# Kernel tuning notes

Measured on AMD Instinct MI355X. Metric: run time of the kernel, lower is better.

Reference implementation:

```python
import jax, jax.numpy as jnp
import numpy as np

NUM_HEADS = 12
HIDDEN = 768
HEAD = HIDDEN // NUM_HEADS
SCALE = HIDDEN ** (-0.5)  # NB: module scales by hidden_dim**-0.5, not head_size**-0.5


def setup_inputs() -> dict:
    key = jax.random.key(0)
    ks = jax.random.split(key, 8)
    B, N = 16, 512
    std = HIDDEN ** (-0.5)
    return {
        "x": jax.random.normal(ks[0], (B, N, HIDDEN), dtype=jnp.float32),
        "encoding_bias": jax.random.normal(ks[1], (B, N, N), dtype=jnp.float32),
        "Wq": jax.random.normal(ks[2], (HIDDEN, HIDDEN), dtype=jnp.float32) * std,
        "Wk": jax.random.normal(ks[3], (HIDDEN, HIDDEN), dtype=jnp.float32) * std,
        "Wv": jax.random.normal(ks[4], (HIDDEN, HIDDEN), dtype=jnp.float32) * std,
        "bv": jax.random.normal(ks[5], (HIDDEN,), dtype=jnp.float32) * 0.01,
        "Wo": jax.random.normal(ks[6], (HIDDEN, HIDDEN), dtype=jnp.float32) * std,
        "bo": jax.random.normal(ks[7], (HIDDEN,), dtype=jnp.float32) * 0.01,
    }


def reference(x, encoding_bias, Wq, Wk, Wv, bv, Wo, bo):
    B, N, _ = x.shape
    # torch nn.Linear: y = x @ W.T (+ b)
    q = (x @ Wq.T).reshape(B, N, NUM_HEADS, HEAD)
    k = (x @ Wk.T).reshape(B, N, NUM_HEADS, HEAD)
    v = (x @ Wv.T + bv).reshape(B, N, NUM_HEADS, HEAD)
    # scores: [B, H, N, N] with additive graph bias broadcast over heads
    a = jnp.einsum("bnhd,bmhd->bhnm", q, k) * SCALE + encoding_bias[:, None, :, :]
    # data-dependent pad mask: rows whose scores are identically zero
    pad_mask = jnp.all(a == 0, axis=-1)  # [B, H, N]
    a = jnp.where(pad_mask[..., None], -jnp.inf, a)
    a = jax.nn.softmax(a, axis=-1)
    a = jnp.nan_to_num(a)  # all -inf rows -> NaN -> 0
    o = jnp.einsum("bhnm,bmhd->bnhd", a, v).reshape(B, N, HIDDEN)
    # dropout is identity in eval mode
    return o @ Wo.T + bo
```

## Files before the change

kernel.cpp:

```cpp
#include <hip/hip_runtime.h>
#include <stdint.h>

typedef unsigned short u16;
typedef unsigned int u32;
typedef __bf16 bf16x8 __attribute__((ext_vector_type(8)));
typedef float f32x4 __attribute__((ext_vector_type(4)));

#define NH 12
#define HD 64
#define SEQ 512
#define BATCH 16
#define HID 768
#define SCALE_Q 0.03608439182435161f

__device__ __forceinline__ u16 f2bf(float f) {
    u32 u = __builtin_bit_cast(u32, f);
    u32 r = (u + 0x7FFFu + ((u >> 16) & 1u)) >> 16;
    return (u16)r;
}
__device__ __forceinline__ float bf2f(u16 h) {
    return __builtin_bit_cast(float, (u32)h << 16);
}

__device__ __forceinline__ void gl2lds16(const u16* g, u16* lds_base) {
    __builtin_amdgcn_global_load_lds(
        (const __attribute__((address_space(1))) u32*)g,
        (__attribute__((address_space(3))) u32*)lds_base, 16, 0, 0);
}

#define NXB 6144
#define NEB 4096
#define NWB 576
__global__ void cvt_all(const float* __restrict__ x, const float* __restrict__ eb,
                        const float* __restrict__ w0, const float* __restrict__ w1,
                        const float* __restrict__ w2, const float* __restrict__ w3,
                        u16* __restrict__ dst) {
    int b = blockIdx.x;
    const float* s; int sb;
    if (b < NXB) { s = x; sb = 0; }
    else if (b < NXB + NEB) { s = eb; sb = NXB; }
    else if (b < NXB + NEB + NWB) { s = w0; sb = NXB + NEB; }
    else if (b < NXB + NEB + 2 * NWB) { s = w1; sb = NXB + NEB + NWB; }
    else if (b < NXB + NEB + 3 * NWB) { s = w2; sb = NXB + NEB + 2 * NWB; }
    else { s = w3; sb = NXB + NEB + 3 * NWB; }
    int li = (b - sb) * 1024 + threadIdx.x * 4;
    float4 v = *(const float4*)(s + li);
    ushort4 o;
    o.x = f2bf(v.x); o.y = f2bf(v.y); o.z = f2bf(v.z); o.w = f2bf(v.w);
    *(ushort4*)(dst + (size_t)b * 1024 + threadIdx.x * 4) = o;
}

__device__ __forceinline__ void stage_gemm(
    const u16* __restrict__ Ag, const u16* __restrict__ Bg, int k0,
    u16* As, u16* Bs, int r0, int q0, int r1, int q1, int w)
{
    gl2lds16(Ag + (size_t)r0 * HID + k0 + q0, As + w * 512);
    gl2lds16(Ag + (size_t)r1 * HID + k0 + q1, As + 2048 + w * 512);
    gl2lds16(Bg + (size_t)r0 * HID + k0 + q0, Bs + w * 512);
    gl2lds16(Bg + (size_t)r1 * HID + k0 + q1, Bs + 2048 + w * 512);
}

__device__ __forceinline__ void gemm_mainloop(
    const u16* __restrict__ Ag, const u16* __restrict__ Bg,
    u16 (*As)[128 * 32], u16 (*Bs)[128 * 32], f32x4 (&acc)[4][4])
{
    const int tid = threadIdx.x;
    const int l = tid & 63, w = tid >> 6;
    const int wm = w & 1, wn = w >> 1;
    const int lr = l & 15, lg = l >> 4;

    const int c0 = tid, c1 = tid + 256;
    const int r0 = c0 >> 2, q0 = (((c0 & 3) ^ ((r0 >> 1) & 3)) * 8);
    const int r1 = c1 >> 2, q1 = (((c1 & 3) ^ ((r1 >> 1) & 3)) * 8);

    const int sA = (lg ^ ((lr >> 1) & 3)) * 8;

    stage_gemm(Ag, Bg, 0, As[0], Bs[0], r0, q0, r1, q1, w);
    stage_gemm(Ag, Bg, 32, As[1], Bs[1], r0, q0, r1, q1, w);

    int cur = 0;
    for (int i = 0; i < 24; i++) {
        if (i < 23)
            asm volatile("s_waitcnt vmcnt(4) lgkmcnt(0)" ::: "memory");
        else
            asm volatile("s_waitcnt vmcnt(0) lgkmcnt(0)" ::: "memory");
        __builtin_amdgcn_s_barrier();
        __builtin_amdgcn_sched_barrier(0);

        int nxt = cur + 2; if (nxt >= 3) nxt -= 3;
        if (i < 22)
            stage_gemm(Ag, Bg, (i + 2) * 32, As[nxt], Bs[nxt], r0, q0, r1, q1, w);

        bf16x8 af[4], bfr[4];
#pragma unroll
        for (int mi = 0; mi < 4; mi++)
            af[mi] = *(const bf16x8*)(As[cur] + (wm * 64 + mi * 16 + lr) * 32 + sA);
#pragma unroll
        for (int ni = 0; ni < 4; ni++)
            bfr[ni] = *(const bf16x8*)(Bs[cur] + (wn * 64 + ni * 16 + lr) * 32 + sA);
#pragma unroll
        for (int mi = 0; mi < 4; mi++)
#pragma unroll
            for (int ni = 0; ni < 4; ni++)
                acc[mi][ni] = __builtin_amdgcn_mfma_f32_16x16x32_bf16(af[mi], bfr[ni], acc[mi][ni], 0, 0, 0);

        cur += 1; if (cur >= 3) cur -= 3;
    }
}

__global__ __launch_bounds__(256, 3) void gemm_qkv(
    const u16* __restrict__ xb, const u16* __restrict__ wq,
    const u16* __restrict__ wk, const u16* __restrict__ wv,
    const float* __restrict__ bv,
    u16* __restrict__ qtb, u16* __restrict__ kb, u16* __restrict__ vtb)
{
    __shared__ __align__(16) u16 As[3][128 * 32];
    __shared__ __align__(16) u16 Bs[3][128 * 32];
    const int tid = threadIdx.x;
    const int l = tid & 63, w = tid >> 6;
    const int wm = w & 1, wn = w >> 1;
    const int lr = l & 15, lg = l >> 4;

    const int L = blockIdx.x;
    const int xcd = L & 7, s = L >> 3;
    const int z = s / 48;
    const int s2 = s - z * 48;
    const int nt = s2 >> 3;
    const int mt = xcd * 8 + (s2 & 7);

    const u16* Bw = (z == 0) ? wq : (z == 1) ? wk : wv;
    const u16* Ag = xb + (size_t)(mt * 128) * HID;
    const u16* Bg = Bw + (size_t)(nt * 128) * HID;

    f32x4 acc[4][4] = {};
    gemm_mainloop(Ag, Bg, As, Bs, acc);

    const float sc = (z == 0) ? SCALE_Q : 1.0f;
#pragma unroll
    for (int mi = 0; mi < 4; mi++) {
#pragma unroll
        for (int ni = 0; ni < 4; ni++) {
            const int jg = nt * 128 + wn * 64 + ni * 16 + lr;
            const int h = jg >> 6, d = jg & 63;
            const int i0 = mt * 128 + wm * 64 + mi * 16 + lg * 4;
            const int b = i0 >> 9, n0 = i0 & 511;
            if (z == 1) {
#pragma unroll
                for (int r2 = 0; r2 < 4; r2++)
                    kb[((size_t)(b * NH + h) * SEQ + n0 + r2) * HD + d] = f2bf(acc[mi][ni][r2]);
            } else {
                float bb = (z == 2) ? bv[jg] : 0.0f;
                ushort4 pk;
                pk.x = f2bf(fmaf(acc[mi][ni][0], sc, bb));
                pk.y = f2bf(fmaf(acc[mi][ni][1], sc, bb));
                pk.z = f2bf(fmaf(acc[mi][ni][2], sc, bb));
                pk.w = f2bf(fmaf(acc[mi][ni][3], sc, bb));
                u16* O = (z == 0) ? qtb : vtb;
                *(ushort4*)(O + ((size_t)(b * NH + h) * HD + d) * SEQ + n0) = pk;
            }
        }
    }
}

__global__ __launch_bounds__(256, 3) void gemm_out(
    const u16* __restrict__ A, const u16* __restrict__ wo,
    const float* __restrict__ bo, float* __restrict__ Cout)
{
    __shared__ __align__(16) u16 As[3][128 * 32];
    __shared__ __align__(16) u16 Bs[3][128 * 32];
    const int tid = threadIdx.x;
    const int l = tid & 63, w = tid >> 6;
    const int wm = w & 1, wn = w >> 1;
    const int lr = l & 15, lg = l >> 4;

    const int L = blockIdx.x;
    const int xcd = L & 7, s = L >> 3;
    const int nt = s >> 3;
    const int mt = xcd * 8 + (s & 7);

    const u16* Ag = A + (size_t)(mt * 128) * HID;
    const u16* Bg = wo + (size_t)(nt * 128) * HID;

    f32x4 acc[4][4] = {};
    gemm_mainloop(Ag, Bg, As, Bs, acc);

#pragma unroll
    for (int mi = 0; mi < 4; mi++) {
#pragma unroll
        for (int ni = 0; ni < 4; ni++) {
            const int jg = nt * 128 + wn * 64 + ni * 16 + lr;
            float bb = bo[jg];
#pragma unroll
            for (int r2 = 0; r2 < 4; r2++) {
                int ig = mt * 128 + wm * 64 + mi * 16 + lg * 4 + r2;
                Cout[(size_t)ig * HID + jg] = acc[mi][ni][r2] + bb;
            }
        }
    }
}

__device__ __forceinline__ void stage_kv(
    const u16* __restrict__ Kg, const u16* __restrict__ Vg, int mt0,
    u16* Ksb, u16* Vsb, int kr0, int kc0, int kr1, int kc1, int w)
{
    gl2lds16(Kg + (size_t)(mt0 + kr0) * HD + kc0 * 8, Ksb + w * 512);
    gl2lds16(Kg + (size_t)(mt0 + kr1) * HD + kc1 * 8, Ksb + 2048 + w * 512);
    gl2lds16(Vg + (size_t)kr0 * SEQ + mt0 + kc0 * 8, Vsb + w * 512);
    gl2lds16(Vg + (size_t)kr1 * SEQ + mt0 + kc1 * 8, Vsb + 2048 + w * 512);
}

__global__ __launch_bounds__(256, 4) void attn_kernel(
    const u16* __restrict__ qtb, const u16* __restrict__ kb, const u16* __restrict__ vtb,
    const u16* __restrict__ ebb, u16* __restrict__ ob)
{
    __shared__ __align__(16) u16 Ks[2][64 * 64];
    __shared__ __align__(16) u16 Vs[2][64 * 64];
    __shared__ __align__(16) u16 Ps[4][16 * 64];

    const int tid = threadIdx.x;
    const int l = tid & 63, w = tid >> 6;
    const int lr = l & 15, lg = l >> 4;

    const int L = blockIdx.x;
    const int xcd = L & 7, s = L >> 3;
    const int b = xcd * 2 + (s / 96);
    const int s2 = s % 96;
    const int h = s2 >> 3, qt = s2 & 7;

    const int bh = b * NH + h;
    const int qrow0 = qt * 64 + w * 16;

    const u16* Kg = kb + (size_t)bh * SEQ * HD;
    const u16* Vg = vtb + (size_t)bh * HD * SEQ;
    const u16* Eg = ebb + ((size_t)b * SEQ + qrow0 + lg * 4) * SEQ;

    const int p0 = tid, p1 = tid + 256;
    const int kr0 = p0 >> 3, kc0 = (p0 & 7) ^ (kr0 & 7);
    const int kr1 = p1 >> 3, kc1 = (p1 & 7) ^ (kr1 & 7);

    stage_kv(Kg, Vg, 0, Ks[0], Vs[0], kr0, kc0, kr1, kc1, w);

    const u16* Qg = qtb + (size_t)bh * HD * SEQ + qrow0 + lr;
    bf16x8 qf0, qf1;
#pragma unroll
    for (int j = 0; j < 8; j++) {
        qf0[j] = __builtin_bit_cast(__bf16, Qg[(size_t)(lg * 8 + j) * SEQ]);
        qf1[j] = __builtin_bit_cast(__bf16, Qg[(size_t)(lg * 8 + j + 32) * SEQ]);
    }

    bf16x8 ones;
#pragma unroll
    for (int j = 0; j < 8; j++) ones[j] = __builtin_bit_cast(__bf16, (u16)0x3F80);

    f32x4 oacc[4] = {};
    f32x4 lacc = {};
    float amax[4] = {0.f, 0.f, 0.f, 0.f};

    for (int t = 0; t < 8; t++) {
        const int cur = t & 1;
        const int mt0 = t * 64;
        __syncthreads();

        u16 bl[4][4];
#pragma unroll
        for (int mi = 0; mi < 4; mi++)
#pragma unroll
            for (int r = 0; r < 4; r++)
                bl[mi][r] = Eg[(size_t)r * SEQ + mt0 + mi * 16 + lr];

        if (t < 7)
            stage_kv(Kg, Vg, mt0 + 64, Ks[cur ^ 1], Vs[cur ^ 1], kr0, kc0, kr1, kc1, w);

        float sm[4][4];
#pragma unroll
        for (int mi = 0; mi < 4; mi++) {
            const int row = mi * 16 + lr;
            bf16x8 kf0 = *(const bf16x8*)(Ks[cur] + row * 64 + ((lg ^ (row & 7)) * 8));
            bf16x8 kf1 = *(const bf16x8*)(Ks[cur] + row * 64 + (((4 + lg) ^ (row & 7)) * 8));
            f32x4 s;
#pragma unroll
            for (int r = 0; r < 4; r++) s[r] = bf2f(bl[mi][r]);
            s = __builtin_amdgcn_mfma_f32_16x16x32_bf16(qf0, kf0, s, 0, 0, 0);
            s = __builtin_amdgcn_mfma_f32_16x16x32_bf16(qf1, kf1, s, 0, 0, 0);
#pragma unroll
            for (int r = 0; r < 4; r++) {
                float sv = s[r];
                amax[r] = fmaxf(amax[r], fabsf(sv));
                sm[mi][r] = __expf(sv);
            }
        }

        u16* Pw = Ps[w];
#pragma unroll
        for (int mi = 0; mi < 4; mi++)
#pragma unroll
            for (int r = 0; r < 4; r++) {
                const int q = lg * 4 + r;
                const int chunk = mi * 2 + (lr >> 3);
                Pw[q * 64 + ((chunk ^ (q & 7)) * 8) + (lr & 7)] = f2bf(sm[mi][r]);
            }

#pragma unroll
        for (int ks = 0; ks < 2; ks++) {
            bf16x8 pf = *(const bf16x8*)(Pw + lr * 64 + (((ks * 4 + lg) ^ (lr & 7)) * 8));
#pragma unroll
            for (int di = 0; di < 4; di++) {
                const int row = di * 16 + lr;
                bf16x8 vf = *(const bf16x8*)(Vs[cur] + row * 64 + (((ks * 4 + lg) ^ (row & 7)) * 8));
                oacc[di] = __builtin_amdgcn_mfma_f32_16x16x32_bf16(pf, vf, oacc[di], 0, 0, 0);
            }
            lacc = __builtin_amdgcn_mfma_f32_16x16x32_bf16(pf, ones, lacc, 0, 0, 0);
        }
    }

#pragma unroll
    for (int r = 0; r < 4; r++) {
        float am = amax[r];
        am = fmaxf(am, __shfl_xor(am, 1));
        am = fmaxf(am, __shfl_xor(am, 2));
        am = fmaxf(am, __shfl_xor(am, 4));
        am = fmaxf(am, __shfl_xor(am, 8));
        float inv = (am > 0.f) ? (1.0f / lacc[r]) : 0.0f;
        int n = qrow0 + lg * 4 + r;
        u16* orow = ob + ((size_t)b * SEQ + n) * HID + h * HD;
#pragma unroll
        for (int di = 0; di < 4; di++)
            orow[di * 16 + lr] = f2bf(oacc[di][r] * inv);
    }
}

extern "C" void kernel_launch(void* const* d_in, const int* in_sizes, int n_in,
                              void* d_out, int out_size, void* d_ws, size_t ws_size,
                              hipStream_t stream) {
    (void)in_sizes; (void)n_in; (void)out_size; (void)ws_size;
    const float* x  = (const float*)d_in[0];
    const float* eb = (const float*)d_in[1];
    const float* Wq = (const float*)d_in[2];
    const float* Wk = (const float*)d_in[3];
    const float* Wv = (const float*)d_in[4];
    const float* bv = (const float*)d_in[5];
    const float* Wo = (const float*)d_in[6];
    const float* bo = (const float*)d_in[7];
    float* out = (float*)d_out;

    const int NX = BATCH * SEQ * HID;
    const int NW = HID * HID;
    const int NE = BATCH * SEQ * SEQ;
    u16* ws   = (u16*)d_ws;
    u16* xb   = ws;
    u16* ebb  = xb + NX;
    u16* wqb  = ebb + NE;
    u16* wkb  = wqb + NW;
    u16* wvb  = wkb + NW;
    u16* wob  = wvb + NW;
    u16* qtb  = wob + NW;
    u16* kb   = qtb + NX;
    u16* vtb  = kb + NX;
    u16* obuf = vtb + NX;

    cvt_all<<<NXB + NEB + 4 * NWB, 256, 0, stream>>>(x, eb, Wq, Wk, Wv, Wo, ws);

    gemm_qkv<<<1152, 256, 0, stream>>>(xb, wqb, wkb, wvb, bv, qtb, kb, vtb);

    attn_kernel<<<1536, 256, 0, stream>>>(qtb, kb, vtb, ebb, obuf);

    gemm_out<<<384, 256, 0, stream>>>(obuf, wob, bo, out);
}
```

Baseline: 201.3 us.

## Transpose score MFMA, vectorize bias loads, replace ones-MFMA row sum with register sum

The attention kernel now computes S^T by swapping the MFMA operands. Each lane then holds one query row, so the bias loads become vectorized ushort4 reads, and the row sum and abs-max are kept in scalar registers instead of an extra MFMA against a ones vector. P is packed with v_cvt_pk_bf16_f32 and written as uint2, and setprio hints wrap the MFMA groups. The QKV GEMM drops its XCD-aware block swizzle for a plain 3D grid, which may lose L2 locality. The intent is to cut MFMA, conversion and global-load instruction overhead in the attention inner loop.

```diff
diff --git a/kernel.cpp b/kernel.cpp
--- a/kernel.cpp
+++ b/kernel.cpp
@@ -20,6 +20,11 @@
 }
 __device__ __forceinline__ float bf2f(u16 h) {
     return __builtin_bit_cast(float, (u32)h << 16);
+}
+__device__ __forceinline__ u32 cvtpk_bf16(float a, float b) {
+    u32 d;
+    asm("v_cvt_pk_bf16_f32 %0, %1, %2" : "=v"(d) : "v"(a), "v"(b));
+    return d;
 }
 
 __device__ __forceinline__ void gl2lds16(const u16* g, u16* lds_base) {
@@ -120,13 +125,7 @@
     const int l = tid & 63, w = tid >> 6;
     const int wm = w & 1, wn = w >> 1;
     const int lr = l & 15, lg = l >> 4;
-
-    const int L = blockIdx.x;
-    const int xcd = L & 7, s = L >> 3;
-    const int z = s / 48;
-    const int s2 = s - z * 48;
-    const int nt = s2 >> 3;
-    const int mt = xcd * 8 + (s2 & 7);
+    const int mt = blockIdx.x, nt = blockIdx.y, z = blockIdx.z;
 
     const u16* Bw = (z == 0) ? wq : (z == 1) ? wk : wv;
     const u16* Ag = xb + (size_t)(mt * 128) * HID;
@@ -232,7 +231,7 @@
 
     const u16* Kg = kb + (size_t)bh * SEQ * HD;
     const u16* Vg = vtb + (size_t)bh * HD * SEQ;
-    const u16* Eg = ebb + ((size_t)b * SEQ + qrow0 + lg * 4) * SEQ;
+    const u16* Eg = ebb + ((size_t)b * SEQ + qrow0 + lr) * SEQ;
 
     const int p0 = tid, p1 = tid + 256;
     const int kr0 = p0 >> 3, kc0 = (p0 & 7) ^ (kr0 & 7);
@@ -248,25 +247,20 @@
         qf1[j] = __builtin_bit_cast(__bf16, Qg[(size_t)(lg * 8 + j + 32) * SEQ]);
     }
 
-    bf16x8 ones;
-#pragma unroll
-    for (int j = 0; j < 8; j++) ones[j] = __builtin_bit_cast(__bf16, (u16)0x3F80);
-
     f32x4 oacc[4] = {};
-    f32x4 lacc = {};
-    float amax[4] = {0.f, 0.f, 0.f, 0.f};
+    float psum = 0.f;
+    float amax = 0.f;
+    u16* Pw = Ps[w];
 
     for (int t = 0; t < 8; t++) {
         const int cur = t & 1;
         const int mt0 = t * 64;
         __syncthreads();
 
-        u16 bl[4][4];
+        ushort4 bl4[4];
 #pragma unroll
         for (int mi = 0; mi < 4; mi++)
-#pragma unroll
-            for (int r = 0; r < 4; r++)
-                bl[mi][r] = Eg[(size_t)r * SEQ + mt0 + mi * 16 + lr];
+            bl4[mi] = *(const ushort4*)(Eg + mt0 + mi * 16 + lg * 4);
 
         if (t < 7)
             stage_kv(Kg, Vg, mt0 + 64, Ks[cur ^ 1], Vs[cur ^ 1], kr0, kc0, kr1, kc1, w);
@@ -277,55 +271,65 @@
             const int row = mi * 16 + lr;
             bf16x8 kf0 = *(const bf16x8*)(Ks[cur] + row * 64 + ((lg ^ (row & 7)) * 8));
             bf16x8 kf1 = *(const bf16x8*)(Ks[cur] + row * 64 + (((4 + lg) ^ (row & 7)) * 8));
-            f32x4 s;
-#pragma unroll
-            for (int r = 0; r < 4; r++) s[r] = bf2f(bl[mi][r]);
-            s = __builtin_amdgcn_mfma_f32_16x16x32_bf16(qf0, kf0, s, 0, 0, 0);
-            s = __builtin_amdgcn_mfma_f32_16x16x32_bf16(qf1, kf1, s, 0, 0, 0);
+            f32x4 sacc;
+            sacc[0] = bf2f(bl4[mi].x); sacc[1] = bf2f(bl4[mi].y);
+            sacc[2] = bf2f(bl4[mi].z); sacc[3] = bf2f(bl4[mi].w);
+            __builtin_amdgcn_s_setprio(1);
+            sacc = __builtin_amdgcn_mfma_f32_16x16x32_bf16(kf0, qf0, sacc, 0, 0, 0);
+            sacc = __builtin_amdgcn_mfma_f32_16x16x32_bf16(kf1, qf1, sacc, 0, 0, 0);
+            __builtin_amdgcn_s_setprio(0);
 #pragma unroll
             for (int r = 0; r < 4; r++) {
-                float sv = s[r];
-                amax[r] = fmaxf(amax[r], fabsf(sv));
-                sm[mi][r] = __expf(sv);
+                float sv = sacc[r];
+                amax = fmaxf(amax, fabsf(sv));
+                float e = __expf(sv);
+                sm[mi][r] = e;
+                psum += e;
             }
         }
 
-        u16* Pw = Ps[w];
-#pragma unroll
-        for (int mi = 0; mi < 4; mi++)
-#pragma unroll
-            for (int r = 0; r < 4; r++) {
-                const int q = lg * 4 + r;
-                const int chunk = mi * 2 + (lr >> 3);
-                Pw[q * 64 + ((chunk ^ (q & 7)) * 8) + (lr & 7)] = f2bf(sm[mi][r]);
-            }
+#pragma unroll
+        for (int mi = 0; mi < 4; mi++) {
+            uint2 pk2;
+            pk2.x = cvtpk_bf16(sm[mi][0], sm[mi][1]);
+            pk2.y = cvtpk_bf16(sm[mi][2], sm[mi][3]);
+            const int slot = (mi * 4 + lg) ^ (lr & 7);
+            *(uint2*)(Pw + lr * 64 + slot * 4) = pk2;
+        }
 
 #pragma unroll
         for (int ks = 0; ks < 2; ks++) {
-            bf16x8 pf = *(const bf16x8*)(Pw + lr * 64 + (((ks * 4 + lg) ^ (lr & 7)) * 8));
+            const int sa = (2 * ks + (lg >> 1)) * 4 + 2 * (lg & 1);
+            uint2 va = *(const uint2*)(Pw + lr * 64 + ((sa ^ (lr & 7)) * 4));
+            uint2 vb = *(const uint2*)(Pw + lr * 64 + (((sa + 1) ^ (lr & 7)) * 4));
+            union { u32 u[4]; bf16x8 v; } pu;
+            pu.u[0] = va.x; pu.u[1] = va.y; pu.u[2] = vb.x; pu.u[3] = vb.y;
+            bf16x8 pf = pu.v;
+            __builtin_amdgcn_s_setprio(1);
 #pragma unroll
             for (int di = 0; di < 4; di++) {
                 const int row = di * 16 + lr;
                 bf16x8 vf = *(const bf16x8*)(Vs[cur] + row * 64 + (((ks * 4 + lg) ^ (row & 7)) * 8));
                 oacc[di] = __builtin_amdgcn_mfma_f32_16x16x32_bf16(pf, vf, oacc[di], 0, 0, 0);
             }
-            lacc = __builtin_amdgcn_mfma_f32_16x16x32_bf16(pf, ones, lacc, 0, 0, 0);
-        }
-    }
+            __builtin_amdgcn_s_setprio(0);
+        }
+    }
+
+    psum += __shfl_xor(psum, 16);
+    psum += __shfl_xor(psum, 32);
+    amax = fmaxf(amax, __shfl_xor(amax, 16));
+    amax = fmaxf(amax, __shfl_xor(amax, 32));
+    float inv = (amax > 0.f) ? (1.0f / psum) : 0.0f;
 
 #pragma unroll
     for (int r = 0; r < 4; r++) {
-        float am = amax[r];
-        am = fmaxf(am, __shfl_xor(am, 1));
-        am = fmaxf(am, __shfl_xor(am, 2));
-        am = fmaxf(am, __shfl_xor(am, 4));
-        am = fmaxf(am, __shfl_xor(am, 8));
-        float inv = (am > 0.f) ? (1.0f / lacc[r]) : 0.0f;
+        float invq = __shfl(inv, lg * 4 + r);
         int n = qrow0 + lg * 4 + r;
         u16* orow = ob + ((size_t)b * SEQ + n) * HID + h * HD;
 #pragma unroll
         for (int di = 0; di < 4; di++)
-            orow[di * 16 + lr] = f2bf(oacc[di][r] * inv);
+            orow[di * 16 + lr] = f2bf(oacc[di][r] * invq);
     }
 }
 
@@ -360,7 +364,7 @@
 
     cvt_all<<<NXB + NEB + 4 * NWB, 256, 0, stream>>>(x, eb, Wq, Wk, Wv, Wo, ws);
 
-    gemm_qkv<<<1152, 256, 0, stream>>>(xb, wqb, wkb, wvb, bv, qtb, kb, vtb);
+    gemm_qkv<<<dim3(64, 6, 3), 256, 0, stream>>>(xb, wqb, wkb, wvb, bv, qtb, kb, vtb);
 
     attn_kernel<<<1536, 256, 0, stream>>>(qtb, kb, vtb, ebb, obuf);
 
```

Result: slower. 209.9 us (+4.3%).

## Transpose encoding bias during bf16 conversion for vectorized attention bias loads

Applied to the files above, without the earlier changes.

Moves conversion of the encoding bias out of the generic cvt_all kernel into a new LDS-tiled kernel that writes it transposed (key-major). This lets the attention kernel fetch four query rows of bias with one 8-byte load per lane instead of four scalar strided 2-byte loads. It also drops the XCD-aware block remapping in gemm_qkv in favor of a plain 3D grid, which may hurt L2 locality. It adds an extra kernel launch, and the transposing kernel's LDS reads may suffer bank conflicts.

```diff
diff --git a/kernel.cpp b/kernel.cpp
--- a/kernel.cpp
+++ b/kernel.cpp
@@ -29,25 +29,54 @@
 }
 
 #define NXB 6144
-#define NEB 4096
 #define NWB 576
-__global__ void cvt_all(const float* __restrict__ x, const float* __restrict__ eb,
+__global__ void cvt_all(const float* __restrict__ x,
                         const float* __restrict__ w0, const float* __restrict__ w1,
                         const float* __restrict__ w2, const float* __restrict__ w3,
                         u16* __restrict__ dst) {
     int b = blockIdx.x;
     const float* s; int sb;
     if (b < NXB) { s = x; sb = 0; }
-    else if (b < NXB + NEB) { s = eb; sb = NXB; }
-    else if (b < NXB + NEB + NWB) { s = w0; sb = NXB + NEB; }
-    else if (b < NXB + NEB + 2 * NWB) { s = w1; sb = NXB + NEB + NWB; }
-    else if (b < NXB + NEB + 3 * NWB) { s = w2; sb = NXB + NEB + 2 * NWB; }
-    else { s = w3; sb = NXB + NEB + 3 * NWB; }
+    else if (b < NXB + NWB) { s = w0; sb = NXB; }
+    else if (b < NXB + 2 * NWB) { s = w1; sb = NXB + NWB; }
+    else if (b < NXB + 3 * NWB) { s = w2; sb = NXB + 2 * NWB; }
+    else { s = w3; sb = NXB + 3 * NWB; }
     int li = (b - sb) * 1024 + threadIdx.x * 4;
     float4 v = *(const float4*)(s + li);
     ushort4 o;
     o.x = f2bf(v.x); o.y = f2bf(v.y); o.z = f2bf(v.z); o.w = f2bf(v.w);
     *(ushort4*)(dst + (size_t)b * 1024 + threadIdx.x * 4) = o;
+}
+
+__global__ void cvt_tr_e(const float* __restrict__ eb, u16* __restrict__ ebt) {
+    __shared__ u16 t[64][66];
+    const int bb = blockIdx.z;
+    const int qt0 = blockIdx.x * 64;
+    const int kt0 = blockIdx.y * 64;
+    const int tid = threadIdx.x;
+    const int r = tid >> 2;
+    const int c4 = (tid & 3) * 16;
+
+    const float* src = eb + ((size_t)bb * SEQ + qt0 + r) * SEQ + kt0 + c4;
+#pragma unroll
+    for (int j = 0; j < 4; j++) {
+        float4 v = *(const float4*)(src + j * 4);
+        t[r][c4 + j * 4 + 0] = f2bf(v.x);
+        t[r][c4 + j * 4 + 1] = f2bf(v.y);
+        t[r][c4 + j * 4 + 2] = f2bf(v.z);
+        t[r][c4 + j * 4 + 3] = f2bf(v.w);
+    }
+    __syncthreads();
+    u16* dst = ebt + ((size_t)bb * SEQ + kt0 + r) * SEQ + qt0 + c4;
+#pragma unroll
+    for (int j = 0; j < 4; j++) {
+        ushort4 o;
+        o.x = t[c4 + j * 4 + 0][r];
+        o.y = t[c4 + j * 4 + 1][r];
+        o.z = t[c4 + j * 4 + 2][r];
+        o.w = t[c4 + j * 4 + 3][r];
+        *(ushort4*)(dst + j * 4) = o;
+    }
 }
 
 __device__ __forceinline__ void stage_gemm(
@@ -120,13 +149,7 @@
     const int l = tid & 63, w = tid >> 6;
     const int wm = w & 1, wn = w >> 1;
     const int lr = l & 15, lg = l >> 4;
-
-    const int L = blockIdx.x;
-    const int xcd = L & 7, s = L >> 3;
-    const int z = s / 48;
-    const int s2 = s - z * 48;
-    const int nt = s2 >> 3;
-    const int mt = xcd * 8 + (s2 & 7);
+    const int mt = blockIdx.x, nt = blockIdx.y, z = blockIdx.z;
 
     const u16* Bw = (z == 0) ? wq : (z == 1) ? wk : wv;
     const u16* Ag = xb + (size_t)(mt * 128) * HID;
@@ -211,7 +234,7 @@
 
 __global__ __launch_bounds__(256, 4) void attn_kernel(
     const u16* __restrict__ qtb, const u16* __restrict__ kb, const u16* __restrict__ vtb,
-    const u16* __restrict__ ebb, u16* __restrict__ ob)
+    const u16* __restrict__ ebt, u16* __restrict__ ob)
 {
     __shared__ __align__(16) u16 Ks[2][64 * 64];
     __shared__ __align__(16) u16 Vs[2][64 * 64];
@@ -232,7 +255,7 @@
 
     const u16* Kg = kb + (size_t)bh * SEQ * HD;
     const u16* Vg = vtb + (size_t)bh * HD * SEQ;
-    const u16* Eg = ebb + ((size_t)b * SEQ + qrow0 + lg * 4) * SEQ;
+    const u16* Egt = ebt + (size_t)b * SEQ * SEQ;
 
     const int p0 = tid, p1 = tid + 256;
     const int kr0 = p0 >> 3, kc0 = (p0 & 7) ^ (kr0 & 7);
@@ -261,12 +284,10 @@
         const int mt0 = t * 64;
         __syncthreads();
 
-        u16 bl[4][4];
+        ushort4 bl4[4];
 #pragma unroll
         for (int mi = 0; mi < 4; mi++)
-#pragma unroll
-            for (int r = 0; r < 4; r++)
-                bl[mi][r] = Eg[(size_t)r * SEQ + mt0 + mi * 16 + lr];
+            bl4[mi] = *(const ushort4*)(Egt + (size_t)(mt0 + mi * 16 + lr) * SEQ + qrow0 + lg * 4);
 
         if (t < 7)
             stage_kv(Kg, Vg, mt0 + 64, Ks[cur ^ 1], Vs[cur ^ 1], kr0, kc0, kr1, kc1, w);
@@ -278,8 +299,8 @@
             bf16x8 kf0 = *(const bf16x8*)(Ks[cur] + row * 64 + ((lg ^ (row & 7)) * 8));
             bf16x8 kf1 = *(const bf16x8*)(Ks[cur] + row * 64 + (((4 + lg) ^ (row & 7)) * 8));
             f32x4 s;
-#pragma unroll
-            for (int r = 0; r < 4; r++) s[r] = bf2f(bl[mi][r]);
+            s[0] = bf2f(bl4[mi].x); s[1] = bf2f(bl4[mi].y);
+            s[2] = bf2f(bl4[mi].z); s[3] = bf2f(bl4[mi].w);
             s = __builtin_amdgcn_mfma_f32_16x16x32_bf16(qf0, kf0, s, 0, 0, 0);
             s = __builtin_amdgcn_mfma_f32_16x16x32_bf16(qf1, kf1, s, 0, 0, 0);
 #pragma unroll
@@ -348,21 +369,23 @@
     const int NE = BATCH * SEQ * SEQ;
     u16* ws   = (u16*)d_ws;
     u16* xb   = ws;
-    u16* ebb  = xb + NX;
-    u16* wqb  = ebb + NE;
+    u16* wqb  = xb + NX;
     u16* wkb  = wqb + NW;
     u16* wvb  = wkb + NW;
     u16* wob  = wvb + NW;
-    u16* qtb  = wob + NW;
+    u16* ebt  = wob + NW;
+    u16* qtb  = ebt + NE;
     u16* kb   = qtb + NX;
     u16* vtb  = kb + NX;
     u16* obuf = vtb + NX;
 
-    cvt_all<<<NXB + NEB + 4 * NWB, 256, 0, stream>>>(x, eb, Wq, Wk, Wv, Wo, ws);
-
-    gemm_qkv<<<1152, 256, 0, stream>>>(xb, wqb, wkb, wvb, bv, qtb, kb, vtb);
-
-    attn_kernel<<<1536, 256, 0, stream>>>(qtb, kb, vtb, ebb, obuf);
+    cvt_all<<<NXB + 4 * NWB, 256, 0, stream>>>(x, Wq, Wk, Wv, Wo, ws);
+
+    cvt_tr_e<<<dim3(8, 8, 16), 256, 0, stream>>>(eb, ebt);
+
+    gemm_qkv<<<dim3(64, 6, 3), 256, 0, stream>>>(xb, wqb, wkb, wvb, bv, qtb, kb, vtb);
+
+    attn_kernel<<<1536, 256, 0, stream>>>(qtb, kb, vtb, ebt, obuf);
 
     gemm_out<<<384, 256, 0, stream>>>(obuf, wob, bo, out);
 }
```

New measurement: 215.2 us. 1.07x slower.

## Read fp32 encoding bias directly in attention and use plain 3D grid for QKV GEMM

Applied to the files above, without the earlier changes.

Drops the separate bf16 conversion of the encoding bias. The attention kernel now loads the fp32 bias straight from the input, which removes a full read and write pass over a 16x512x512 tensor in the conversion kernel. The cost is that attention reads twice as many bytes of bias per tile. The QKV GEMM launch also switches from an XCD-aware swizzled 1D grid to a simple 3D grid, which may change L2 locality across chiplets.

```diff
diff --git a/kernel.cpp b/kernel.cpp
--- a/kernel.cpp
+++ b/kernel.cpp
@@ -29,20 +29,18 @@
 }
 
 #define NXB 6144
-#define NEB 4096
 #define NWB 576
-__global__ void cvt_all(const float* __restrict__ x, const float* __restrict__ eb,
+__global__ void cvt_all(const float* __restrict__ x,
                         const float* __restrict__ w0, const float* __restrict__ w1,
                         const float* __restrict__ w2, const float* __restrict__ w3,
                         u16* __restrict__ dst) {
     int b = blockIdx.x;
     const float* s; int sb;
     if (b < NXB) { s = x; sb = 0; }
-    else if (b < NXB + NEB) { s = eb; sb = NXB; }
-    else if (b < NXB + NEB + NWB) { s = w0; sb = NXB + NEB; }
-    else if (b < NXB + NEB + 2 * NWB) { s = w1; sb = NXB + NEB + NWB; }
-    else if (b < NXB + NEB + 3 * NWB) { s = w2; sb = NXB + NEB + 2 * NWB; }
-    else { s = w3; sb = NXB + NEB + 3 * NWB; }
+    else if (b < NXB + NWB) { s = w0; sb = NXB; }
+    else if (b < NXB + 2 * NWB) { s = w1; sb = NXB + NWB; }
+    else if (b < NXB + 3 * NWB) { s = w2; sb = NXB + 2 * NWB; }
+    else { s = w3; sb = NXB + 3 * NWB; }
     int li = (b - sb) * 1024 + threadIdx.x * 4;
     float4 v = *(const float4*)(s + li);
     ushort4 o;
@@ -120,13 +118,7 @@
     const int l = tid & 63, w = tid >> 6;
     const int wm = w & 1, wn = w >> 1;
     const int lr = l & 15, lg = l >> 4;
-
-    const int L = blockIdx.x;
-    const int xcd = L & 7, s = L >> 3;
-    const int z = s / 48;
-    const int s2 = s - z * 48;
-    const int nt = s2 >> 3;
-    const int mt = xcd * 8 + (s2 & 7);
+    const int mt = blockIdx.x, nt = blockIdx.y, z = blockIdx.z;
 
     const u16* Bw = (z == 0) ? wq : (z == 1) ? wk : wv;
     const u16* Ag = xb + (size_t)(mt * 128) * HID;
@@ -211,7 +203,7 @@
 
 __global__ __launch_bounds__(256, 4) void attn_kernel(
     const u16* __restrict__ qtb, const u16* __restrict__ kb, const u16* __restrict__ vtb,
-    const u16* __restrict__ ebb, u16* __restrict__ ob)
+    const float* __restrict__ eb, u16* __restrict__ ob)
 {
     __shared__ __align__(16) u16 Ks[2][64 * 64];
     __shared__ __align__(16) u16 Vs[2][64 * 64];
@@ -232,7 +224,7 @@
 
     const u16* Kg = kb + (size_t)bh * SEQ * HD;
     const u16* Vg = vtb + (size_t)bh * HD * SEQ;
-    const u16* Eg = ebb + ((size_t)b * SEQ + qrow0 + lg * 4) * SEQ;
+    const float* Eg = eb + ((size_t)b * SEQ + qrow0 + lg * 4) * SEQ;
 
     const int p0 = tid, p1 = tid + 256;
     const int kr0 = p0 >> 3, kc0 = (p0 & 7) ^ (kr0 & 7);
@@ -261,7 +253,7 @@
         const int mt0 = t * 64;
         __syncthreads();
 
-        u16 bl[4][4];
+        float bl[4][4];
 #pragma unroll
         for (int mi = 0; mi < 4; mi++)
 #pragma unroll
@@ -279,7 +271,7 @@
             bf16x8 kf1 = *(const bf16x8*)(Ks[cur] + row * 64 + (((4 + lg) ^ (row & 7)) * 8));
             f32x4 s;
 #pragma unroll
-            for (int r = 0; r < 4; r++) s[r] = bf2f(bl[mi][r]);
+            for (int r = 0; r < 4; r++) s[r] = bl[mi][r];
             s = __builtin_amdgcn_mfma_f32_16x16x32_bf16(qf0, kf0, s, 0, 0, 0);
             s = __builtin_amdgcn_mfma_f32_16x16x32_bf16(qf1, kf1, s, 0, 0, 0);
 #pragma unroll
@@ -345,11 +337,9 @@
 
     const int NX = BATCH * SEQ * HID;
     const int NW = HID * HID;
-    const int NE = BATCH * SEQ * SEQ;
     u16* ws   = (u16*)d_ws;
     u16* xb   = ws;
-    u16* ebb  = xb + NX;
-    u16* wqb  = ebb + NE;
+    u16* wqb  = xb + NX;
     u16* wkb  = wqb + NW;
     u16* wvb  = wkb + NW;
     u16* wob  = wvb + NW;
@@ -358,11 +348,11 @@
     u16* vtb  = kb + NX;
     u16* obuf = vtb + NX;
 
-    cvt_all<<<NXB + NEB + 4 * NWB, 256, 0, stream>>>(x, eb, Wq, Wk, Wv, Wo, ws);
-
-    gemm_qkv<<<1152, 256, 0, stream>>>(xb, wqb, wkb, wvb, bv, qtb, kb, vtb);
-
-    attn_kernel<<<1536, 256, 0, stream>>>(qtb, kb, vtb, ebb, obuf);
+    cvt_all<<<NXB + 4 * NWB, 256, 0, stream>>>(x, Wq, Wk, Wv, Wo, ws);
+
+    gemm_qkv<<<dim3(64, 6, 3), 256, 0, stream>>>(xb, wqb, wkb, wvb, bv, qtb, kb, vtb);
+
+    attn_kernel<<<1536, 256, 0, stream>>>(qtb, kb, vtb, eb, obuf);
 
     gemm_out<<<384, 256, 0, stream>>>(obuf, wob, bo, out);
 }
```

New measurement: 200.3 us. No clear change (-0.5%).
